# Kernel optimization log

Hardware: AMD Instinct MI355X
Metric: run time of the kernel (lower is better)

## Reference

```python
import jax, jax.numpy as jnp
import numpy as np

N_EMBD = 1024
N_HEAD = 16
HEAD_DIM = N_EMBD // N_HEAD


def setup_inputs() -> dict:
    key = jax.random.key(0)
    k1, k2, k3, k4, k5 = jax.random.split(key, 5)
    scale = 1.0 / np.sqrt(N_EMBD)
    x = jax.random.normal(k1, (4, 2048, N_EMBD), dtype=jnp.float32)
    W_qkv = jax.random.normal(k2, (N_EMBD, 3 * N_EMBD), dtype=jnp.float32) * scale
    b_qkv = jax.random.normal(k3, (3 * N_EMBD,), dtype=jnp.float32) * 0.01
    W_proj = jax.random.normal(k4, (N_EMBD, N_EMBD), dtype=jnp.float32) * scale
    b_proj = jax.random.normal(k5, (N_EMBD,), dtype=jnp.float32) * 0.01
    return {"x": x, "W_qkv": W_qkv, "b_qkv": b_qkv, "W_proj": W_proj, "b_proj": b_proj}


def reference(x, W_qkv, b_qkv, W_proj, b_proj):
    B, T, C = x.shape
    qkv = x @ W_qkv + b_qkv                      # [B,T,3C]
    q, k, v = jnp.split(qkv, 3, axis=-1)
    # [B,T,C] -> [B,H,T,D]
    def to_heads(t):
        return t.reshape(B, T, N_HEAD, HEAD_DIM).transpose(0, 2, 1, 3)
    q, k, v = to_heads(q), to_heads(k), to_heads(v)
    att = jnp.einsum('bhqd,bhkd->bhqk', q, k) / np.sqrt(HEAD_DIM)
    causal = jnp.tril(jnp.ones((T, T), dtype=bool))
    att = jnp.where(causal, att, -jnp.inf)
    att = jax.nn.softmax(att, axis=-1)
    y = jnp.einsum('bhqk,bhkd->bhqd', att, v)    # [B,H,T,D]
    y = y.transpose(0, 2, 1, 3).reshape(B, T, C)
    return y @ W_proj + b_proj
```

## Files before the change

### kernel.cpp

```cpp
#include <hip/hip_runtime.h>
#include <hip/hip_bf16.h>
#include <cstdint>

#define B_   4
#define T_   2048
#define C_   1024
#define H_   16
#define D_   64
#define TC3  3072
#define M_   (B_ * T_)

typedef short  bf16x8 __attribute__((ext_vector_type(8)));
typedef float  f32x4  __attribute__((ext_vector_type(4)));

#define AS1(p) ((const __attribute__((address_space(1))) void*)(p))
#define AS3(p) ((__attribute__((address_space(3))) void*)(p))

__device__ inline unsigned short f2bf(float f) {
    union { float f; unsigned int i; } x; x.f = f;
    return (unsigned short)((x.i + 0x7fffu + ((x.i >> 16) & 1u)) >> 16);
}

__global__ void cast_f32_bf16(const float* __restrict__ in,
                              unsigned short* __restrict__ out) {
    const size_t i = ((size_t)blockIdx.x * blockDim.x + threadIdx.x) * 8;
    f32x4 a = *(const f32x4*)(in + i);
    f32x4 b = *(const f32x4*)(in + i + 4);
    bf16x8 o;
#pragma unroll
    for (int j = 0; j < 4; ++j) { o[j] = (short)f2bf(a[j]); o[4 + j] = (short)f2bf(b[j]); }
    *(bf16x8*)(out + i) = o;
}

__global__ void transpose_cast(const float* __restrict__ in,
                               unsigned short* __restrict__ out, int R, int C) {
    __shared__ unsigned short tile[32][33];
    const int bc = blockIdx.x * 32, br = blockIdx.y * 32;
    const int tx = threadIdx.x & 31, ty = threadIdx.x >> 5;
#pragma unroll
    for (int i = 0; i < 4; ++i) {
        int r = ty + i * 8;
        tile[r][tx] = f2bf(in[(size_t)(br + r) * C + bc + tx]);
    }
    __syncthreads();
#pragma unroll
    for (int i = 0; i < 4; ++i) {
        int r = ty + i * 8;
        out[(size_t)(bc + r) * R + br + tx] = tile[tx][r];
    }
}

template <bool OUTF32>
__global__ __launch_bounds__(256, 2) void gemm_bt_bias(
    const unsigned short* __restrict__ A, const unsigned short* __restrict__ Bt,
    const float* __restrict__ bias, void* __restrict__ Cout,
    int M, int N, int K) {
    __shared__ unsigned short As[128 * 32];
    __shared__ unsigned short Bs[128 * 32];
    const int tid = threadIdx.x;
    const int wave = tid >> 6, lane = tid & 63;
    const int m0 = blockIdx.x * 128, n0 = blockIdx.y * 128;
    const int wr = (wave >> 1) * 64, wc = (wave & 1) * 64;

    f32x4 acc[4][4] = {};

    const int srow = (lane >> 2);
    const int scol = (lane & 3) * 8;

    for (int k0 = 0; k0 < K; k0 += 32) {
#pragma unroll
        for (int j = 0; j < 2; ++j) {
            const int chunk = wave * 2 + j;
            const int row = chunk * 16 + srow;
            __builtin_amdgcn_global_load_lds(
                AS1(A + (size_t)(m0 + row) * K + k0 + scol),
                AS3(As + chunk * 512), 16, 0, 0);
            __builtin_amdgcn_global_load_lds(
                AS1(Bt + (size_t)(n0 + row) * K + k0 + scol),
                AS3(Bs + chunk * 512), 16, 0, 0);
        }
        __syncthreads();
        bf16x8 a[4], b[4];
#pragma unroll
        for (int i = 0; i < 4; ++i)
            a[i] = *(const bf16x8*)&As[(wr + i * 16 + (lane & 15)) * 32 + (lane >> 4) * 8];
#pragma unroll
        for (int i = 0; i < 4; ++i)
            b[i] = *(const bf16x8*)&Bs[(wc + i * 16 + (lane & 15)) * 32 + (lane >> 4) * 8];
        __builtin_amdgcn_s_setprio(1);
#pragma unroll
        for (int i = 0; i < 4; ++i)
#pragma unroll
            for (int j = 0; j < 4; ++j)
                acc[i][j] = __builtin_amdgcn_mfma_f32_16x16x32_bf16(a[i], b[j], acc[i][j], 0, 0, 0);
        __builtin_amdgcn_s_setprio(0);
        __syncthreads();
    }

#pragma unroll
    for (int i = 0; i < 4; ++i) {
        const int rowb = m0 + wr + i * 16 + (lane >> 4) * 4;
#pragma unroll
        for (int j = 0; j < 4; ++j) {
            const int col = n0 + wc + j * 16 + (lane & 15);
            const float bv = bias[col];
#pragma unroll
            for (int r = 0; r < 4; ++r) {
                const float v = acc[i][j][r] + bv;
                if (OUTF32)
                    ((float*)Cout)[(size_t)(rowb + r) * N + col] = v;
                else
                    ((unsigned short*)Cout)[(size_t)(rowb + r) * N + col] = f2bf(v);
            }
        }
    }
}

__global__ __launch_bounds__(256, 2) void attn_kernel(
    const unsigned short* __restrict__ QKV, unsigned short* __restrict__ Y) {
    __shared__ unsigned short Kl[64][72];
    __shared__ unsigned int   Vt32[64][36];
    __shared__ unsigned short Pl[4][32][72];

    const int tid = threadIdx.x, wave = tid >> 6, lane = tid & 63;
    const int bh = blockIdx.x;
    const int pr = blockIdx.y;
    const int b = bh >> 4, h = bh & 15;
    const size_t rowbase = (size_t)b * T_ * TC3;
    const int l15 = lane & 15, lhi = lane >> 4;
    const int sk2 = tid >> 3;
    const int sseg = tid & 7;

    for (int sp = 0; sp < 2; ++sp) {
        const int tq = sp ? (15 - pr) : pr;
        const int qb = tq * 128;
        const int q0 = qb + wave * 32;
        const int ntiles = 2 * tq + 2;

        bf16x8 qf[2][2];
#pragma unroll
        for (int mi = 0; mi < 2; ++mi) {
            const unsigned short* p =
                QKV + rowbase + (size_t)(q0 + mi * 16 + l15) * TC3 + h * 64 + lhi * 8;
            qf[mi][0] = *(const bf16x8*)p;
            qf[mi][1] = *(const bf16x8*)(p + 32);
        }

        float m_run[2][4], l_run[2][4];
        f32x4 o[2][4] = {};
#pragma unroll
        for (int mi = 0; mi < 2; ++mi)
#pragma unroll
            for (int r = 0; r < 4; ++r) { m_run[mi][r] = -1e30f; l_run[mi][r] = 0.f; }

        __syncthreads();
        {
            const unsigned short* src =
                QKV + rowbase + (size_t)(2 * sk2) * TC3 + C_ + h * 64 + sseg * 8;
            bf16x8 ka = *(const bf16x8*)src;
            bf16x8 kb = *(const bf16x8*)(src + TC3);
            bf16x8 va = *(const bf16x8*)(src + C_);
            bf16x8 vb = *(const bf16x8*)(src + C_ + TC3);
            *(bf16x8*)&Kl[2 * sk2][sseg * 8] = ka;
            *(bf16x8*)&Kl[2 * sk2 + 1][sseg * 8] = kb;
            const int kx = sk2 ^ (sseg << 2);
#pragma unroll
            for (int j = 0; j < 8; ++j)
                Vt32[sseg * 8 + j][kx] =
                    (unsigned int)(unsigned short)va[j] |
                    ((unsigned int)(unsigned short)vb[j] << 16);
        }

        for (int t = 0; t < ntiles; ++t) {
            const int kv0 = t * 64;
            __syncthreads();

            bf16x8 pka, pkb, pva, pvb;
            const bool pf_valid = (t + 1 < ntiles);
            if (pf_valid) {
                const unsigned short* src =
                    QKV + rowbase + (size_t)(kv0 + 64 + 2 * sk2) * TC3 + C_ + h * 64 + sseg * 8;
                pka = *(const bf16x8*)src;
                pkb = *(const bf16x8*)(src + TC3);
                pva = *(const bf16x8*)(src + C_);
                pvb = *(const bf16x8*)(src + C_ + TC3);
            }

            if (q0 + 31 >= kv0) {
                f32x4 s[2][4];
                __builtin_amdgcn_s_setprio(1);
#pragma unroll
                for (int kt = 0; kt < 4; ++kt) {
                    bf16x8 kf0 = *(const bf16x8*)&Kl[kt * 16 + l15][lhi * 8];
                    bf16x8 kf1 = *(const bf16x8*)&Kl[kt * 16 + l15][32 + lhi * 8];
#pragma unroll
                    for (int mi = 0; mi < 2; ++mi) {
                        f32x4 acc = {};
                        acc = __builtin_amdgcn_mfma_f32_16x16x32_bf16(qf[mi][0], kf0, acc, 0, 0, 0);
                        acc = __builtin_amdgcn_mfma_f32_16x16x32_bf16(qf[mi][1], kf1, acc, 0, 0, 0);
                        s[mi][kt] = acc;
                    }
                }
                __builtin_amdgcn_s_setprio(0);

                const bool needmask = (kv0 + 63 > q0);
#pragma unroll
                for (int mi = 0; mi < 2; ++mi) {
                    if (needmask) {
#pragma unroll
                        for (int kt = 0; kt < 4; ++kt) {
                            const int kcol = kv0 + kt * 16 + l15;
#pragma unroll
                            for (int r = 0; r < 4; ++r) {
                                const int q = q0 + mi * 16 + lhi * 4 + r;
                                const float v = s[mi][kt][r] * 0.125f;
                                s[mi][kt][r] = (kcol <= q) ? v : -1e30f;
                            }
                        }
                    } else {
#pragma unroll
                        for (int kt = 0; kt < 4; ++kt)
#pragma unroll
                            for (int r = 0; r < 4; ++r)
                                s[mi][kt][r] *= 0.125f;
                    }
                    float tmax[4];
#pragma unroll
                    for (int r = 0; r < 4; ++r)
                        tmax[r] = fmaxf(fmaxf(s[mi][0][r], s[mi][1][r]),
                                        fmaxf(s[mi][2][r], s[mi][3][r]));
#pragma unroll
                    for (int msk = 1; msk < 16; msk <<= 1)
#pragma unroll
                        for (int r = 0; r < 4; ++r)
                            tmax[r] = fmaxf(tmax[r], __shfl_xor(tmax[r], msk, 64));

                    bool exc = false;
#pragma unroll
                    for (int r = 0; r < 4; ++r)
                        exc = exc || (tmax[r] > m_run[mi][r] + 8.0f);
                    if (__any(exc)) {
#pragma unroll
                        for (int r = 0; r < 4; ++r) {
                            const float mnew = fmaxf(m_run[mi][r], tmax[r]);
                            const float corr = __expf(m_run[mi][r] - mnew);
                            m_run[mi][r] = mnew;
                            l_run[mi][r] *= corr;
#pragma unroll
                            for (int dt = 0; dt < 4; ++dt) o[mi][dt][r] *= corr;
                        }
                    }
                    float tsum[4] = {0.f, 0.f, 0.f, 0.f};
#pragma unroll
                    for (int kt = 0; kt < 4; ++kt)
#pragma unroll
                        for (int r = 0; r < 4; ++r) {
                            const float p = __expf(s[mi][kt][r] - m_run[mi][r]);
                            s[mi][kt][r] = p;
                            tsum[r] += p;
                        }
#pragma unroll
                    for (int msk = 1; msk < 16; msk <<= 1)
#pragma unroll
                        for (int r = 0; r < 4; ++r)
                            tsum[r] += __shfl_xor(tsum[r], msk, 64);
#pragma unroll
                    for (int r = 0; r < 4; ++r) l_run[mi][r] += tsum[r];

#pragma unroll
                    for (int kt = 0; kt < 4; ++kt)
#pragma unroll
                        for (int r = 0; r < 4; ++r)
                            Pl[wave][mi * 16 + lhi * 4 + r][kt * 16 + l15] = f2bf(s[mi][kt][r]);
                }

                bf16x8 pf[2][2];
#pragma unroll
                for (int mi = 0; mi < 2; ++mi) {
                    pf[mi][0] = *(const bf16x8*)&Pl[wave][mi * 16 + l15][lhi * 8];
                    pf[mi][1] = *(const bf16x8*)&Pl[wave][mi * 16 + l15][32 + lhi * 8];
                }
                __builtin_amdgcn_s_setprio(1);
#pragma unroll
                for (int dt = 0; dt < 4; ++dt) {
                    const int d = dt * 16 + l15;
                    const int s4 = (d >> 3) << 2;
                    bf16x8 vf0 = *(const bf16x8*)&Vt32[d][(lhi * 4) ^ s4];
                    bf16x8 vf1 = *(const bf16x8*)&Vt32[d][(16 + lhi * 4) ^ s4];
#pragma unroll
                    for (int mi = 0; mi < 2; ++mi) {
                        o[mi][dt] = __builtin_amdgcn_mfma_f32_16x16x32_bf16(pf[mi][0], vf0, o[mi][dt], 0, 0, 0);
                        o[mi][dt] = __builtin_amdgcn_mfma_f32_16x16x32_bf16(pf[mi][1], vf1, o[mi][dt], 0, 0, 0);
                    }
                }
                __builtin_amdgcn_s_setprio(0);
            }

            __syncthreads();
            if (pf_valid) {
                *(bf16x8*)&Kl[2 * sk2][sseg * 8] = pka;
                *(bf16x8*)&Kl[2 * sk2 + 1][sseg * 8] = pkb;
                const int kx = sk2 ^ (sseg << 2);
#pragma unroll
                for (int j = 0; j < 8; ++j)
                    Vt32[sseg * 8 + j][kx] =
                        (unsigned int)(unsigned short)pva[j] |
                        ((unsigned int)(unsigned short)pvb[j] << 16);
            }
        }

#pragma unroll
        for (int mi = 0; mi < 2; ++mi)
#pragma unroll
            for (int dt = 0; dt < 4; ++dt)
#pragma unroll
                for (int r = 0; r < 4; ++r) {
                    const int q = q0 + mi * 16 + lhi * 4 + r;
                    const int d = dt * 16 + l15;
                    Y[((size_t)b * T_ + q) * C_ + h * 64 + d] = f2bf(o[mi][dt][r] / l_run[mi][r]);
                }
    }
}

extern "C" void kernel_launch(void* const* d_in, const int* in_sizes, int n_in,
                              void* d_out, int out_size, void* d_ws, size_t ws_size,
                              hipStream_t stream) {
    const float* x     = (const float*)d_in[0];
    const float* Wqkv  = (const float*)d_in[1];
    const float* bqkv  = (const float*)d_in[2];
    const float* Wproj = (const float*)d_in[3];
    const float* bproj = (const float*)d_in[4];
    float* out = (float*)d_out;

    char* ws = (char*)d_ws;
    unsigned short* qkv    = (unsigned short*)(ws);
    unsigned short* yat    = (unsigned short*)(ws + 50331648);
    unsigned short* WqkvT  = (unsigned short*)(ws + 67108864);
    unsigned short* WprojT = (unsigned short*)(ws + 73400320);
    unsigned short* xb     = (unsigned short*)(ws + 75497472);

    cast_f32_bf16<<<dim3((M_ * C_) / (256 * 8)), dim3(256), 0, stream>>>(x, xb);
    transpose_cast<<<dim3(TC3 / 32, C_ / 32), dim3(256), 0, stream>>>(Wqkv, WqkvT, C_, TC3);
    transpose_cast<<<dim3(C_ / 32, C_ / 32), dim3(256), 0, stream>>>(Wproj, WprojT, C_, C_);
    gemm_bt_bias<false><<<dim3(M_ / 128, TC3 / 128), dim3(256), 0, stream>>>(xb, WqkvT, bqkv, qkv, M_, TC3, C_);
    attn_kernel<<<dim3(B_ * H_, 8), dim3(256), 0, stream>>>(qkv, yat);
    gemm_bt_bias<true><<<dim3(M_ / 128, C_ / 128), dim3(256), 0, stream>>>(yat, WprojT, bproj, out, M_, C_, C_);
}
```

Before: 225.2 us.

## Launch one attention block per query tile, pre-scale Q, pack V with perm

The attention kernel previously paired a short and a long query tile in each block (grid 64x8). It now launches one block per query tile (grid 64x16), with blockIdx.y reversed so the heaviest tiles start first, and raises launch_bounds occupancy from 2 to 4 blocks. Q is multiplied by 1/sqrt(D) once at load time, so the per-tile score scaling goes away, at the cost of an extra bf16 rounding on Q. The V transpose packing now uses v_perm byte permutes instead of shifts and ORs. The aim is finer-grained scheduling and higher occupancy, but the higher launch bound may squeeze registers and cause spills.

```diff
diff --git a/kernel.cpp b/kernel.cpp
--- a/kernel.cpp
+++ b/kernel.cpp
@@ -16,6 +16,9 @@
 #define AS1(p) ((const __attribute__((address_space(1))) void*)(p))
 #define AS3(p) ((__attribute__((address_space(3))) void*)(p))
 
+__device__ inline float bf2f(unsigned short u) {
+    union { unsigned int i; float f; } x; x.i = ((unsigned int)u) << 16; return x.f;
+}
 __device__ inline unsigned short f2bf(float f) {
     union { float f; unsigned int i; } x; x.f = f;
     return (unsigned short)((x.i + 0x7fffu + ((x.i >> 16) & 1u)) >> 16);
@@ -116,7 +119,17 @@
     }
 }
 
-__global__ __launch_bounds__(256, 2) void attn_kernel(
+__device__ inline void pack_v_pair(const bf16x8& va, const bf16x8& vb, unsigned int* dst) {
+    const unsigned int* a32 = (const unsigned int*)&va;
+    const unsigned int* b32 = (const unsigned int*)&vb;
+#pragma unroll
+    for (int j2 = 0; j2 < 4; ++j2) {
+        dst[2 * j2]     = __builtin_amdgcn_perm(b32[j2], a32[j2], 0x05040100u);
+        dst[2 * j2 + 1] = __builtin_amdgcn_perm(b32[j2], a32[j2], 0x07060302u);
+    }
+}
+
+__global__ __launch_bounds__(256, 4) void attn_kernel(
     const unsigned short* __restrict__ QKV, unsigned short* __restrict__ Y) {
     __shared__ unsigned short Kl[64][72];
     __shared__ unsigned int   Vt32[64][36];
@@ -124,202 +137,194 @@
 
     const int tid = threadIdx.x, wave = tid >> 6, lane = tid & 63;
     const int bh = blockIdx.x;
-    const int pr = blockIdx.y;
+    const int tq = 15 - (int)blockIdx.y;
     const int b = bh >> 4, h = bh & 15;
     const size_t rowbase = (size_t)b * T_ * TC3;
     const int l15 = lane & 15, lhi = lane >> 4;
     const int sk2 = tid >> 3;
     const int sseg = tid & 7;
 
-    for (int sp = 0; sp < 2; ++sp) {
-        const int tq = sp ? (15 - pr) : pr;
-        const int qb = tq * 128;
-        const int q0 = qb + wave * 32;
-        const int ntiles = 2 * tq + 2;
-
-        bf16x8 qf[2][2];
-#pragma unroll
-        for (int mi = 0; mi < 2; ++mi) {
-            const unsigned short* p =
-                QKV + rowbase + (size_t)(q0 + mi * 16 + l15) * TC3 + h * 64 + lhi * 8;
-            qf[mi][0] = *(const bf16x8*)p;
-            qf[mi][1] = *(const bf16x8*)(p + 32);
-        }
-
-        float m_run[2][4], l_run[2][4];
-        f32x4 o[2][4] = {};
-#pragma unroll
-        for (int mi = 0; mi < 2; ++mi)
-#pragma unroll
-            for (int r = 0; r < 4; ++r) { m_run[mi][r] = -1e30f; l_run[mi][r] = 0.f; }
-
+    const int qb = tq * 128;
+    const int q0 = qb + wave * 32;
+    const int ntiles = 2 * tq + 2;
+
+    bf16x8 qf[2][2];
+#pragma unroll
+    for (int mi = 0; mi < 2; ++mi) {
+        const unsigned short* p =
+            QKV + rowbase + (size_t)(q0 + mi * 16 + l15) * TC3 + h * 64 + lhi * 8;
+        qf[mi][0] = *(const bf16x8*)p;
+        qf[mi][1] = *(const bf16x8*)(p + 32);
+#pragma unroll
+        for (int hf = 0; hf < 2; ++hf)
+#pragma unroll
+            for (int j = 0; j < 8; ++j)
+                qf[mi][hf][j] = (short)f2bf(bf2f((unsigned short)qf[mi][hf][j]) * 0.125f);
+    }
+
+    float m_run[2][4], l_run[2][4];
+    f32x4 o[2][4] = {};
+#pragma unroll
+    for (int mi = 0; mi < 2; ++mi)
+#pragma unroll
+        for (int r = 0; r < 4; ++r) { m_run[mi][r] = -1e30f; l_run[mi][r] = 0.f; }
+
+    {
+        const unsigned short* src =
+            QKV + rowbase + (size_t)(2 * sk2) * TC3 + C_ + h * 64 + sseg * 8;
+        bf16x8 ka = *(const bf16x8*)src;
+        bf16x8 kb = *(const bf16x8*)(src + TC3);
+        bf16x8 va = *(const bf16x8*)(src + C_);
+        bf16x8 vb = *(const bf16x8*)(src + C_ + TC3);
+        *(bf16x8*)&Kl[2 * sk2][sseg * 8] = ka;
+        *(bf16x8*)&Kl[2 * sk2 + 1][sseg * 8] = kb;
+        unsigned int pk[8];
+        pack_v_pair(va, vb, pk);
+        const int kx = sk2 ^ (sseg << 2);
+#pragma unroll
+        for (int j = 0; j < 8; ++j) Vt32[sseg * 8 + j][kx] = pk[j];
+    }
+
+    for (int t = 0; t < ntiles; ++t) {
+        const int kv0 = t * 64;
         __syncthreads();
-        {
+
+        bf16x8 pka, pkb, pva, pvb;
+        const bool pf_valid = (t + 1 < ntiles);
+        if (pf_valid) {
             const unsigned short* src =
-                QKV + rowbase + (size_t)(2 * sk2) * TC3 + C_ + h * 64 + sseg * 8;
-            bf16x8 ka = *(const bf16x8*)src;
-            bf16x8 kb = *(const bf16x8*)(src + TC3);
-            bf16x8 va = *(const bf16x8*)(src + C_);
-            bf16x8 vb = *(const bf16x8*)(src + C_ + TC3);
-            *(bf16x8*)&Kl[2 * sk2][sseg * 8] = ka;
-            *(bf16x8*)&Kl[2 * sk2 + 1][sseg * 8] = kb;
-            const int kx = sk2 ^ (sseg << 2);
-#pragma unroll
-            for (int j = 0; j < 8; ++j)
-                Vt32[sseg * 8 + j][kx] =
-                    (unsigned int)(unsigned short)va[j] |
-                    ((unsigned int)(unsigned short)vb[j] << 16);
-        }
-
-        for (int t = 0; t < ntiles; ++t) {
-            const int kv0 = t * 64;
-            __syncthreads();
-
-            bf16x8 pka, pkb, pva, pvb;
-            const bool pf_valid = (t + 1 < ntiles);
-            if (pf_valid) {
-                const unsigned short* src =
-                    QKV + rowbase + (size_t)(kv0 + 64 + 2 * sk2) * TC3 + C_ + h * 64 + sseg * 8;
-                pka = *(const bf16x8*)src;
-                pkb = *(const bf16x8*)(src + TC3);
-                pva = *(const bf16x8*)(src + C_);
-                pvb = *(const bf16x8*)(src + C_ + TC3);
-            }
-
-            if (q0 + 31 >= kv0) {
-                f32x4 s[2][4];
-                __builtin_amdgcn_s_setprio(1);
-#pragma unroll
-                for (int kt = 0; kt < 4; ++kt) {
-                    bf16x8 kf0 = *(const bf16x8*)&Kl[kt * 16 + l15][lhi * 8];
-                    bf16x8 kf1 = *(const bf16x8*)&Kl[kt * 16 + l15][32 + lhi * 8];
-#pragma unroll
-                    for (int mi = 0; mi < 2; ++mi) {
-                        f32x4 acc = {};
-                        acc = __builtin_amdgcn_mfma_f32_16x16x32_bf16(qf[mi][0], kf0, acc, 0, 0, 0);
-                        acc = __builtin_amdgcn_mfma_f32_16x16x32_bf16(qf[mi][1], kf1, acc, 0, 0, 0);
-                        s[mi][kt] = acc;
+                QKV + rowbase + (size_t)(kv0 + 64 + 2 * sk2) * TC3 + C_ + h * 64 + sseg * 8;
+            pka = *(const bf16x8*)src;
+            pkb = *(const bf16x8*)(src + TC3);
+            pva = *(const bf16x8*)(src + C_);
+            pvb = *(const bf16x8*)(src + C_ + TC3);
+        }
+
+        if (q0 + 31 >= kv0) {
+            f32x4 s[2][4];
+            __builtin_amdgcn_s_setprio(1);
+#pragma unroll
+            for (int kt = 0; kt < 4; ++kt) {
+                bf16x8 kf0 = *(const bf16x8*)&Kl[kt * 16 + l15][lhi * 8];
+                bf16x8 kf1 = *(const bf16x8*)&Kl[kt * 16 + l15][32 + lhi * 8];
+#pragma unroll
+                for (int mi = 0; mi < 2; ++mi) {
+                    f32x4 acc = {};
+                    acc = __builtin_amdgcn_mfma_f32_16x16x32_bf16(qf[mi][0], kf0, acc, 0, 0, 0);
+                    acc = __builtin_amdgcn_mfma_f32_16x16x32_bf16(qf[mi][1], kf1, acc, 0, 0, 0);
+                    s[mi][kt] = acc;
+                }
+            }
+            __builtin_amdgcn_s_setprio(0);
+
+            const bool needmask = (kv0 + 63 > q0);
+#pragma unroll
+            for (int mi = 0; mi < 2; ++mi) {
+                if (needmask) {
+#pragma unroll
+                    for (int kt = 0; kt < 4; ++kt) {
+                        const int kcol = kv0 + kt * 16 + l15;
+#pragma unroll
+                        for (int r = 0; r < 4; ++r) {
+                            const int q = q0 + mi * 16 + lhi * 4 + r;
+                            s[mi][kt][r] = (kcol <= q) ? s[mi][kt][r] : -1e30f;
+                        }
                     }
                 }
-                __builtin_amdgcn_s_setprio(0);
-
-                const bool needmask = (kv0 + 63 > q0);
-#pragma unroll
-                for (int mi = 0; mi < 2; ++mi) {
-                    if (needmask) {
-#pragma unroll
-                        for (int kt = 0; kt < 4; ++kt) {
-                            const int kcol = kv0 + kt * 16 + l15;
-#pragma unroll
-                            for (int r = 0; r < 4; ++r) {
-                                const int q = q0 + mi * 16 + lhi * 4 + r;
-                                const float v = s[mi][kt][r] * 0.125f;
-                                s[mi][kt][r] = (kcol <= q) ? v : -1e30f;
-                            }
-                        }
-                    } else {
-#pragma unroll
-                        for (int kt = 0; kt < 4; ++kt)
-#pragma unroll
-                            for (int r = 0; r < 4; ++r)
-                                s[mi][kt][r] *= 0.125f;
-                    }
-                    float tmax[4];
+                float tmax[4];
+#pragma unroll
+                for (int r = 0; r < 4; ++r)
+                    tmax[r] = fmaxf(fmaxf(s[mi][0][r], s[mi][1][r]),
+                                    fmaxf(s[mi][2][r], s[mi][3][r]));
+#pragma unroll
+                for (int msk = 1; msk < 16; msk <<= 1)
 #pragma unroll
                     for (int r = 0; r < 4; ++r)
-                        tmax[r] = fmaxf(fmaxf(s[mi][0][r], s[mi][1][r]),
-                                        fmaxf(s[mi][2][r], s[mi][3][r]));
-#pragma unroll
-                    for (int msk = 1; msk < 16; msk <<= 1)
-#pragma unroll
-                        for (int r = 0; r < 4; ++r)
-                            tmax[r] = fmaxf(tmax[r], __shfl_xor(tmax[r], msk, 64));
-
-                    bool exc = false;
-#pragma unroll
-                    for (int r = 0; r < 4; ++r)
-                        exc = exc || (tmax[r] > m_run[mi][r] + 8.0f);
-                    if (__any(exc)) {
-#pragma unroll
-                        for (int r = 0; r < 4; ++r) {
-                            const float mnew = fmaxf(m_run[mi][r], tmax[r]);
-                            const float corr = __expf(m_run[mi][r] - mnew);
-                            m_run[mi][r] = mnew;
-                            l_run[mi][r] *= corr;
-#pragma unroll
-                            for (int dt = 0; dt < 4; ++dt) o[mi][dt][r] *= corr;
-                        }
-                    }
-                    float tsum[4] = {0.f, 0.f, 0.f, 0.f};
-#pragma unroll
-                    for (int kt = 0; kt < 4; ++kt)
-#pragma unroll
-                        for (int r = 0; r < 4; ++r) {
-                            const float p = __expf(s[mi][kt][r] - m_run[mi][r]);
-                            s[mi][kt][r] = p;
-                            tsum[r] += p;
-                        }
-#pragma unroll
-                    for (int msk = 1; msk < 16; msk <<= 1)
-#pragma unroll
-                        for (int r = 0; r < 4; ++r)
-                            tsum[r] += __shfl_xor(tsum[r], msk, 64);
-#pragma unroll
-                    for (int r = 0; r < 4; ++r) l_run[mi][r] += tsum[r];
-
-#pragma unroll
-                    for (int kt = 0; kt < 4; ++kt)
-#pragma unroll
-                        for (int r = 0; r < 4; ++r)
-                            Pl[wave][mi * 16 + lhi * 4 + r][kt * 16 + l15] = f2bf(s[mi][kt][r]);
-                }
-
-                bf16x8 pf[2][2];
-#pragma unroll
-                for (int mi = 0; mi < 2; ++mi) {
-                    pf[mi][0] = *(const bf16x8*)&Pl[wave][mi * 16 + l15][lhi * 8];
-                    pf[mi][1] = *(const bf16x8*)&Pl[wave][mi * 16 + l15][32 + lhi * 8];
-                }
-                __builtin_amdgcn_s_setprio(1);
-#pragma unroll
-                for (int dt = 0; dt < 4; ++dt) {
-                    const int d = dt * 16 + l15;
-                    const int s4 = (d >> 3) << 2;
-                    bf16x8 vf0 = *(const bf16x8*)&Vt32[d][(lhi * 4) ^ s4];
-                    bf16x8 vf1 = *(const bf16x8*)&Vt32[d][(16 + lhi * 4) ^ s4];
-#pragma unroll
-                    for (int mi = 0; mi < 2; ++mi) {
-                        o[mi][dt] = __builtin_amdgcn_mfma_f32_16x16x32_bf16(pf[mi][0], vf0, o[mi][dt], 0, 0, 0);
-                        o[mi][dt] = __builtin_amdgcn_mfma_f32_16x16x32_bf16(pf[mi][1], vf1, o[mi][dt], 0, 0, 0);
+                        tmax[r] = fmaxf(tmax[r], __shfl_xor(tmax[r], msk, 64));
+
+                bool exc = false;
+#pragma unroll
+                for (int r = 0; r < 4; ++r)
+                    exc = exc || (tmax[r] > m_run[mi][r] + 8.0f);
+                if (__any(exc)) {
+#pragma unroll
+                    for (int r = 0; r < 4; ++r) {
+                        const float mnew = fmaxf(m_run[mi][r], tmax[r]);
+                        const float corr = __expf(m_run[mi][r] - mnew);
+                        m_run[mi][r] = mnew;
+                        l_run[mi][r] *= corr;
+#pragma unroll
+                        for (int dt = 0; dt < 4; ++dt) o[mi][dt][r] *= corr;
                     }
                 }
-                __builtin_amdgcn_s_setprio(0);
-            }
-
-            __syncthreads();
-            if (pf_valid) {
-                *(bf16x8*)&Kl[2 * sk2][sseg * 8] = pka;
-                *(bf16x8*)&Kl[2 * sk2 + 1][sseg * 8] = pkb;
-                const int kx = sk2 ^ (sseg << 2);
-#pragma unroll
-                for (int j = 0; j < 8; ++j)
-                    Vt32[sseg * 8 + j][kx] =
-                        (unsigned int)(unsigned short)pva[j] |
-                        ((unsigned int)(unsigned short)pvb[j] << 16);
-            }
-        }
-
-#pragma unroll
-        for (int mi = 0; mi < 2; ++mi)
-#pragma unroll
-            for (int dt = 0; dt < 4; ++dt)
-#pragma unroll
-                for (int r = 0; r < 4; ++r) {
-                    const int q = q0 + mi * 16 + lhi * 4 + r;
-                    const int d = dt * 16 + l15;
-                    Y[((size_t)b * T_ + q) * C_ + h * 64 + d] = f2bf(o[mi][dt][r] / l_run[mi][r]);
+                float tsum[4] = {0.f, 0.f, 0.f, 0.f};
+#pragma unroll
+                for (int kt = 0; kt < 4; ++kt)
+#pragma unroll
+                    for (int r = 0; r < 4; ++r) {
+                        const float p = __expf(s[mi][kt][r] - m_run[mi][r]);
+                        s[mi][kt][r] = p;
+                        tsum[r] += p;
+                    }
+#pragma unroll
+                for (int msk = 1; msk < 16; msk <<= 1)
+#pragma unroll
+                    for (int r = 0; r < 4; ++r)
+                        tsum[r] += __shfl_xor(tsum[r], msk, 64);
+#pragma unroll
+                for (int r = 0; r < 4; ++r) l_run[mi][r] += tsum[r];
+
+#pragma unroll
+                for (int kt = 0; kt < 4; ++kt)
+#pragma unroll
+                    for (int r = 0; r < 4; ++r)
+                        Pl[wave][mi * 16 + lhi * 4 + r][kt * 16 + l15] = f2bf(s[mi][kt][r]);
+            }
+
+            bf16x8 pf[2][2];
+#pragma unroll
+            for (int mi = 0; mi < 2; ++mi) {
+                pf[mi][0] = *(const bf16x8*)&Pl[wave][mi * 16 + l15][lhi * 8];
+                pf[mi][1] = *(const bf16x8*)&Pl[wave][mi * 16 + l15][32 + lhi * 8];
+            }
+            __builtin_amdgcn_s_setprio(1);
+#pragma unroll
+            for (int dt = 0; dt < 4; ++dt) {
+                const int d = dt * 16 + l15;
+                const int s4 = (d >> 3) << 2;
+                bf16x8 vf0 = *(const bf16x8*)&Vt32[d][(lhi * 4) ^ s4];
+                bf16x8 vf1 = *(const bf16x8*)&Vt32[d][(16 + lhi * 4) ^ s4];
+#pragma unroll
+                for (int mi = 0; mi < 2; ++mi) {
+                    o[mi][dt] = __builtin_amdgcn_mfma_f32_16x16x32_bf16(pf[mi][0], vf0, o[mi][dt], 0, 0, 0);
+                    o[mi][dt] = __builtin_amdgcn_mfma_f32_16x16x32_bf16(pf[mi][1], vf1, o[mi][dt], 0, 0, 0);
                 }
-    }
+            }
+            __builtin_amdgcn_s_setprio(0);
+        }
+
+        __syncthreads();
+        if (pf_valid) {
+            *(bf16x8*)&Kl[2 * sk2][sseg * 8] = pka;
+            *(bf16x8*)&Kl[2 * sk2 + 1][sseg * 8] = pkb;
+            unsigned int pk[8];
+            pack_v_pair(pva, pvb, pk);
+            const int kx = sk2 ^ (sseg << 2);
+#pragma unroll
+            for (int j = 0; j < 8; ++j) Vt32[sseg * 8 + j][kx] = pk[j];
+        }
+    }
+
+#pragma unroll
+    for (int mi = 0; mi < 2; ++mi)
+#pragma unroll
+        for (int dt = 0; dt < 4; ++dt)
+#pragma unroll
+            for (int r = 0; r < 4; ++r) {
+                const int q = q0 + mi * 16 + lhi * 4 + r;
+                const int d = dt * 16 + l15;
+                Y[((size_t)b * T_ + q) * C_ + h * 64 + d] = f2bf(o[mi][dt][r] / l_run[mi][r]);
+            }
 }
 
 extern "C" void kernel_launch(void* const* d_in, const int* in_sizes, int n_in,
@@ -343,6 +348,6 @@
     transpose_cast<<<dim3(TC3 / 32, C_ / 32), dim3(256), 0, stream>>>(Wqkv, WqkvT, C_, TC3);
     transpose_cast<<<dim3(C_ / 32, C_ / 32), dim3(256), 0, stream>>>(Wproj, WprojT, C_, C_);
     gemm_bt_bias<false><<<dim3(M_ / 128, TC3 / 128), dim3(256), 0, stream>>>(xb, WqkvT, bqkv, qkv, M_, TC3, C_);
-    attn_kernel<<<dim3(B_ * H_, 8), dim3(256), 0, stream>>>(qkv, yat);
+    attn_kernel<<<dim3(B_ * H_, 16), dim3(256), 0, stream>>>(qkv, yat);
     gemm_bt_bias<true><<<dim3(M_ / 128, C_ / 128), dim3(256), 0, stream>>>(yat, WprojT, bproj, out, M_, C_, C_);
 }
```

Measured after the change: 270.5 us. 20.1% more time.
